# Performance work log

Hardware: AMD Instinct MI355X
Metric: run time of the kernel (lower is better)

The kernel has to match this reference:

```python
import jax, jax.numpy as jnp
import numpy as np

B, D, NH, HD = 32, 384, 8, 48
HP = WP = 14
N = HP * WP
L = 24
EPS_LN = 1e-5


def _ln(x, w, b):
    m = jnp.mean(x, -1, keepdims=True)
    v = jnp.mean((x - m) ** 2, -1, keepdims=True)
    return (x - m) * jax.lax.rsqrt(v + EPS_LN) * w + b


def _gelu(x):
    return jax.nn.gelu(x, approximate=False)


def _conv(x, w, s, p, groups=1):
    return jax.lax.conv_general_dilated(x, w, (s, s), [(p, p), (p, p)],
        dimension_numbers=('NCHW', 'OIHW', 'NCHW'), feature_group_count=groups)


def _bn(x, g, b):
    # eval-mode BatchNorm2d with running_mean=0, running_var=1
    scale = g * jax.lax.rsqrt(jnp.asarray(1.0 + 1e-5, x.dtype))
    return x * scale[None, :, None, None] + b[None, :, None, None]


def _pos_embed(pos_w, pos_b):
    two_pi = 2.0 * np.pi
    y = (jnp.arange(HP, dtype=jnp.float32) + 1.0) / ((HP + 1e-6) * two_pi)
    xg = (jnp.arange(WP, dtype=jnp.float32) + 1.0) / ((WP + 1e-6) * two_pi)
    y_embed = jnp.broadcast_to(y[:, None], (HP, WP))
    x_embed = jnp.broadcast_to(xg[None, :], (HP, WP))
    dim_t = 10000.0 ** (2.0 * (jnp.arange(32) // 2).astype(jnp.float32) / 32.0)
    px = x_embed[..., None] / dim_t  # [H,W,32]
    py = y_embed[..., None] / dim_t
    px = jnp.stack([jnp.sin(px[..., 0::2]), jnp.cos(px[..., 1::2])], -1).reshape(HP, WP, 32)
    py = jnp.stack([jnp.sin(py[..., 0::2]), jnp.cos(py[..., 1::2])], -1).reshape(HP, WP, 32)
    pos = jnp.concatenate([py, px], -1)  # [H,W,64]
    pos = jnp.einsum('hwc,dc->hwd', pos, pos_w[:, :, 0, 0]) + pos_b
    return pos.reshape(1, N, D)


def _xca_block(t, p):
    Bc = t.shape[0]
    h = _ln(t, p['n1_w'], p['n1_b'])
    qkv = (h @ p['qkv_w'].T + p['qkv_b']).reshape(Bc, N, 3, NH, HD)
    q = qkv[:, :, 0].transpose(0, 2, 3, 1)  # [B,H,d,N]
    k = qkv[:, :, 1].transpose(0, 2, 3, 1)
    v = qkv[:, :, 2].transpose(0, 2, 3, 1)
    q = q / jnp.maximum(jnp.linalg.norm(q, axis=-1, keepdims=True), 1e-12)
    k = k / jnp.maximum(jnp.linalg.norm(k, axis=-1, keepdims=True), 1e-12)
    attn = jnp.einsum('bhdn,bhen->bhde', q, k) * p['temp'][None, :, None, None]
    a = jax.nn.softmax(attn, -1)  # channel-wise softmax over d_h
    o = jnp.einsum('bhde,bhen->bnhd', a, v).reshape(Bc, N, D)
    o = o @ p['proj_w'].T + p['proj_b']
    t = t + p['g1'] * o
    h = _ln(t, p['n3_w'], p['n3_b']).transpose(0, 2, 1).reshape(Bc, D, HP, WP)
    h = _conv(h, p['lpi1_w'], 1, 1, groups=D) + p['lpi1_b'][None, :, None, None]
    h = _bn(_gelu(h), p['lpi_bn_g'], p['lpi_bn_b'])
    h = _conv(h, p['lpi2_w'], 1, 1, groups=D) + p['lpi2_b'][None, :, None, None]
    t = t + p['g3'] * h.reshape(Bc, D, N).transpose(0, 2, 1)
    h = _ln(t, p['n2_w'], p['n2_b'])
    h = _gelu(h @ p['fc1_w'].T + p['fc1_b']) @ p['fc2_w'].T + p['fc2_b']
    return t + p['g2'] * h


def _ca_block(t, p):
    Bc, Nc, _ = t.shape
    h = _ln(t, p['n1_w'], p['n1_b'])
    qkv = (h @ p['qkv_w'].T + p['qkv_b']).reshape(Bc, Nc, 3, NH, HD)
    q = qkv[:, :, 0].transpose(0, 2, 1, 3)  # [B,H,N,d]
    k = qkv[:, :, 1].transpose(0, 2, 1, 3)
    v = qkv[:, :, 2].transpose(0, 2, 1, 3)
    attn = jnp.sum(q[:, :, :1] * k, -1) * (HD ** -0.5)  # [B,H,N]
    a = jax.nn.softmax(attn, -1)
    cls = jnp.einsum('bhn,bhnd->bhd', a, v).reshape(Bc, 1, D)
    cls = cls @ p['proj_w'].T + p['proj_b']
    attn_out = jnp.concatenate([cls, h[:, 1:]], 1)
    t = t + p['g1'] * attn_out
    t = _ln(t, p['n2_w'], p['n2_b'])
    res = t
    cls2 = _gelu(t[:, :1] @ p['fc1_w'].T + p['fc1_b']) @ p['fc2_w'].T + p['fc2_b']
    return jnp.concatenate([p['g2'] * cls2, t[:, 1:]], 1) + res


def setup_inputs() -> dict:
    key = jax.random.key(0)
    k = iter(jax.random.split(key, 64))
    def rn(shape, std=0.02):
        return jax.random.normal(next(k), shape, jnp.float32) * std
    inp = {}
    inp['x'] = jax.random.normal(next(k), (B, 3, 224, 224), jnp.float32)
    inp['cls_token'] = rn((1, 1, D))
    inp['pos_w'] = rn((D, 64, 1, 1))
    inp['pos_b'] = jnp.zeros((D,))
    for i, (co, ci) in enumerate([(48, 3), (96, 48), (192, 96), (384, 192)], 1):
        inp['pe_w%d' % i] = rn((co, ci, 3, 3))
        inp['pe_g%d' % i] = jnp.ones((co,))
        inp['pe_b%d' % i] = jnp.zeros((co,))
    inp['xqkv_w'] = rn((L, 3 * D, D)); inp['xqkv_b'] = jnp.zeros((L, 3 * D))
    inp['xproj_w'] = rn((L, D, D)); inp['xproj_b'] = jnp.zeros((L, D))
    inp['xtemp'] = jnp.ones((L, NH))
    for n in ('n1', 'n2', 'n3'):
        inp['x%s_w' % n] = jnp.ones((L, D)); inp['x%s_b' % n] = jnp.zeros((L, D))
    inp['xfc1_w'] = rn((L, 4 * D, D)); inp['xfc1_b'] = jnp.zeros((L, 4 * D))
    inp['xfc2_w'] = rn((L, D, 4 * D)); inp['xfc2_b'] = jnp.zeros((L, D))
    inp['xlpi1_w'] = rn((L, D, 1, 3, 3), 0.1); inp['xlpi1_b'] = jnp.zeros((L, D))
    inp['xlpi2_w'] = rn((L, D, 1, 3, 3), 0.1); inp['xlpi2_b'] = jnp.zeros((L, D))
    inp['xbn_g'] = jnp.ones((L, D)); inp['xbn_b'] = jnp.zeros((L, D))
    for g in ('g1', 'g2', 'g3'):
        inp['x%s' % g] = jnp.full((L, D), 1e-5)
    L2 = 2
    inp['cqkv_w'] = rn((L2, 3 * D, D)); inp['cqkv_b'] = jnp.zeros((L2, 3 * D))
    inp['cproj_w'] = rn((L2, D, D)); inp['cproj_b'] = jnp.zeros((L2, D))
    for n in ('n1', 'n2'):
        inp['c%s_w' % n] = jnp.ones((L2, D)); inp['c%s_b' % n] = jnp.zeros((L2, D))
    inp['cfc1_w'] = rn((L2, 4 * D, D)); inp['cfc1_b'] = jnp.zeros((L2, 4 * D))
    inp['cfc2_w'] = rn((L2, D, 4 * D)); inp['cfc2_b'] = jnp.zeros((L2, D))
    inp['cg1'] = jnp.full((L2, D), 1e-5); inp['cg2'] = jnp.full((L2, D), 1e-5)
    inp['norm_w'] = jnp.ones((D,)); inp['norm_b'] = jnp.zeros((D,))
    inp['head_w'] = rn((1000, D)); inp['head_b'] = jnp.zeros((1000,))
    return inp


def reference(x, cls_token, pos_w, pos_b, pe_w1, pe_g1, pe_b1, pe_w2, pe_g2, pe_b2, pe_w3, pe_g3, pe_b3, pe_w4, pe_g4, pe_b4, xqkv_w, xqkv_b, xproj_w, xproj_b, xtemp, xn1_w, xn1_b, xn2_w, xn2_b, xn3_w, xn3_b, xfc1_w, xfc1_b, xfc2_w, xfc2_b, xlpi1_w, xlpi1_b, xlpi2_w, xlpi2_b, xbn_g, xbn_b, xg1, xg2, xg3, cqkv_w, cqkv_b, cproj_w, cproj_b, cn1_w, cn1_b, cn2_w, cn2_b, cfc1_w, cfc1_b, cfc2_w, cfc2_b, cg1, cg2, norm_w, norm_b, head_w, head_b):
    h = _gelu(_bn(_conv(x, pe_w1, 2, 1), pe_g1, pe_b1))
    h = _gelu(_bn(_conv(h, pe_w2, 2, 1), pe_g2, pe_b2))
    h = _gelu(_bn(_conv(h, pe_w3, 2, 1), pe_g3, pe_b3))
    h = _bn(_conv(h, pe_w4, 2, 1), pe_g4, pe_b4)  # [B,D,14,14]
    t = h.reshape(h.shape[0], D, N).transpose(0, 2, 1)  # [B,N,D]
    t = t + _pos_embed(pos_w, pos_b)
    xca = {'qkv_w': xqkv_w, 'qkv_b': xqkv_b, 'proj_w': xproj_w, 'proj_b': xproj_b,
           'temp': xtemp, 'n1_w': xn1_w, 'n1_b': xn1_b, 'n2_w': xn2_w, 'n2_b': xn2_b,
           'n3_w': xn3_w, 'n3_b': xn3_b, 'fc1_w': xfc1_w, 'fc1_b': xfc1_b,
           'fc2_w': xfc2_w, 'fc2_b': xfc2_b, 'lpi1_w': xlpi1_w, 'lpi1_b': xlpi1_b,
           'lpi2_w': xlpi2_w, 'lpi2_b': xlpi2_b, 'lpi_bn_g': xbn_g, 'lpi_bn_b': xbn_b,
           'g1': xg1, 'g2': xg2, 'g3': xg3}
    t, _ = jax.lax.scan(lambda c, p: (_xca_block(c, p), None), t, xca)
    t = jnp.concatenate([jnp.broadcast_to(cls_token, (t.shape[0], 1, D)), t], 1)
    for i in range(2):
        p = {'qkv_w': cqkv_w[i], 'qkv_b': cqkv_b[i], 'proj_w': cproj_w[i],
             'proj_b': cproj_b[i], 'n1_w': cn1_w[i], 'n1_b': cn1_b[i],
             'n2_w': cn2_w[i], 'n2_b': cn2_b[i], 'fc1_w': cfc1_w[i],
             'fc1_b': cfc1_b[i], 'fc2_w': cfc2_w[i], 'fc2_b': cfc2_b[i],
             'g1': cg1[i], 'g2': cg2[i]}
        t = _ca_block(t, p)
    t = _ln(t, norm_w, norm_b)[:, 0]
    return t @ head_w.T + head_b
```

## Files before the change

### kernel.cpp

```cpp
#include <hip/hip_runtime.h>
#include <hip/hip_bf16.h>

#define B_ 32
#define D_ 384
#define N_ 196
#define NH_ 8
#define HD_ 48
#define L_ 24

typedef __bf16 bf16x8 __attribute__((ext_vector_type(8)));
typedef __bf16 bf16x4 __attribute__((ext_vector_type(4)));
typedef float f32x4 __attribute__((ext_vector_type(4)));

__device__ __forceinline__ float gelu_f(float v){
    return 0.5f * v * (1.0f + erff(v * 0.70710678118654752f));
}

__global__ __launch_bounds__(256) void cvt_bf(const float* __restrict__ s, __bf16* __restrict__ d, long n){
    long i = ((long)blockIdx.x * 256 + threadIdx.x) * 8;
    if (i >= n) return;
    float4 a = *reinterpret_cast<const float4*>(s + i);
    float4 b = *reinterpret_cast<const float4*>(s + i + 4);
    bf16x8 r;
    r[0] = (__bf16)a.x; r[1] = (__bf16)a.y; r[2] = (__bf16)a.z; r[3] = (__bf16)a.w;
    r[4] = (__bf16)b.x; r[5] = (__bf16)b.y; r[6] = (__bf16)b.z; r[7] = (__bf16)b.w;
    *reinterpret_cast<bf16x8*>(d + i) = r;
}

__global__ __launch_bounds__(256) void cvt_pad(const float* __restrict__ s, __bf16* __restrict__ d,
                                               int rows, int K, int rows_pad){
    int id = blockIdx.x * 256 + threadIdx.x;
    if (id >= rows_pad * K) return;
    int r = id / K;
    d[id] = (r < rows) ? (__bf16)s[id] : (__bf16)0.f;
}

__global__ __launch_bounds__(256) void wprep(const float* __restrict__ w, __bf16* __restrict__ W2,
                                             int Co, int Ci, int Kpad){
    int id = blockIdx.x * 256 + threadIdx.x;
    if (id >= Co * Kpad) return;
    int co = id / Kpad, k = id - co * Kpad;
    float v = 0.f;
    if (k < 9 * Ci){
        int tap = k / Ci, ci = k - tap * Ci;
        v = w[((long)co * Ci + ci) * 9 + tap];
    }
    W2[id] = (__bf16)v;
}

__global__ __launch_bounds__(256) void im2col_x(const float* __restrict__ x, __bf16* __restrict__ A){
    int id = blockIdx.x * 256 + threadIdx.x;
    if (id >= 401408) return;
    int ox = id % 112; int t1 = id / 112; int oy = t1 % 112; int b = t1 / 112;
    __bf16 buf[32];
    #pragma unroll
    for (int i = 0; i < 32; i++) buf[i] = (__bf16)0.f;
    const float* xb = x + (long)b * 3 * 224 * 224;
    #pragma unroll
    for (int tap = 0; tap < 9; tap++){
        int ky = tap / 3, kx = tap % 3;
        int iy = oy * 2 - 1 + ky, ix = ox * 2 - 1 + kx;
        if ((unsigned)iy < 224u && (unsigned)ix < 224u){
            #pragma unroll
            for (int ci = 0; ci < 3; ci++)
                buf[tap * 3 + ci] = (__bf16)xb[((long)ci * 224 + iy) * 224 + ix];
        }
    }
    __bf16* dst = A + (long)id * 32;
    #pragma unroll
    for (int i = 0; i < 4; i++)
        *reinterpret_cast<bf16x8*>(dst + i * 8) = *reinterpret_cast<bf16x8*>(buf + i * 8);
}

__global__ __launch_bounds__(256) void im2col_bf(const __bf16* __restrict__ in, __bf16* __restrict__ A,
                                                 int C, int Hi, int Wi, int Ho, int Wo, int Kpad, int total){
    int id = blockIdx.x * 256 + threadIdx.x;
    if (id >= total) return;
    int tap = id % 9; int pix = id / 9;
    int ox = pix % Wo; int t1 = pix / Wo; int oy = t1 % Ho; int b = t1 / Ho;
    int ky = tap / 3, kx = tap % 3;
    int iy = oy * 2 - 1 + ky, ix = ox * 2 - 1 + kx;
    __bf16* dst = A + (long)pix * Kpad + tap * C;
    if ((unsigned)iy < (unsigned)Hi && (unsigned)ix < (unsigned)Wi){
        const __bf16* src = in + ((long)(b * Hi + iy) * Wi + ix) * C;
        for (int c = 0; c < C; c += 8)
            *reinterpret_cast<bf16x8*>(dst + c) = *reinterpret_cast<const bf16x8*>(src + c);
    } else {
        bf16x8 z{};
        for (int c = 0; c < C; c += 8) *reinterpret_cast<bf16x8*>(dst + c) = z;
    }
    if (tap == 0){
        bf16x8 z{};
        for (int c = 9 * C; c < Kpad; c += 8)
            *reinterpret_cast<bf16x8*>(A + (long)pix * Kpad + c) = z;
    }
}

template<int GELU, int POSOUT>
__global__ __launch_bounds__(256) void gemm_conv(const __bf16* __restrict__ A, int Kpad,
                                                 const __bf16* __restrict__ W,
                                                 const float* __restrict__ g, const float* __restrict__ bb,
                                                 void* __restrict__ Cv, int N,
                                                 const float* __restrict__ pos){
    __shared__ __align__(16) char smem[20480];
    char* Ab = smem;
    char* Bb = smem + 10240;
    const int tid  = threadIdx.x;
    const int lane = tid & 63;
    const int wn   = (tid >> 6) & 1;
    const int wm   = tid >> 7;
    const int row0 = blockIdx.x * 128;
    const int col0 = blockIdx.y * 128;
    const int hi = lane >> 4, lo = lane & 15;
    f32x4 acc[4][4] = {};
    auto loadA = [&](int kk, int i)->bf16x8 {
        int p = i * 256 + tid;
        int r = p >> 2, cq = p & 3;
        return *reinterpret_cast<const bf16x8*>(A + (long)(row0 + r) * Kpad + kk + cq * 8);
    };
    auto loadB = [&](int kk, int i)->bf16x8 {
        int p = i * 256 + tid;
        int r = p >> 2, cq = p & 3;
        int gc = col0 + r;
        bf16x8 vw{};
        if (gc < N) vw = *reinterpret_cast<const bf16x8*>(W + (long)gc * Kpad + kk + cq * 8);
        return vw;
    };
    bf16x8 vaC0 = loadA(0, 0), vaC1 = loadA(0, 1);
    bf16x8 vwC0 = loadB(0, 0), vwC1 = loadB(0, 1);
    for (int k0 = 0; k0 < Kpad; k0 += 32){
        #pragma unroll
        for (int i = 0; i < 2; i++){
            int p = i * 256 + tid;
            int r = p >> 2, cq = p & 3;
            *reinterpret_cast<bf16x8*>(Ab + r * 80 + cq * 16) = i ? vaC1 : vaC0;
            *reinterpret_cast<bf16x8*>(Bb + r * 80 + cq * 16) = i ? vwC1 : vwC0;
        }
        __syncthreads();
        int kn = (k0 + 32 < Kpad) ? k0 + 32 : k0;
        bf16x8 vaN0 = loadA(kn, 0), vaN1 = loadA(kn, 1);
        bf16x8 vwN0 = loadB(kn, 0), vwN1 = loadB(kn, 1);
        bf16x8 af[4], bfr[4];
        #pragma unroll
        for (int m = 0; m < 4; m++)
            af[m] = *reinterpret_cast<const bf16x8*>(Ab + (wm * 64 + m * 16 + lo) * 80 + hi * 16);
        #pragma unroll
        for (int n = 0; n < 4; n++)
            bfr[n] = *reinterpret_cast<const bf16x8*>(Bb + (wn * 64 + n * 16 + lo) * 80 + hi * 16);
        #pragma unroll
        for (int m = 0; m < 4; m++)
            #pragma unroll
            for (int n = 0; n < 4; n++)
                acc[m][n] = __builtin_amdgcn_mfma_f32_16x16x32_bf16(af[m], bfr[n], acc[m][n], 0, 0, 0);
        __syncthreads();
        vaC0 = vaN0; vaC1 = vaN1; vwC0 = vwN0; vwC1 = vwN1;
    }
    float* Cf = (float*)Cv;
    __bf16* Cb = (__bf16*)Cv;
    #pragma unroll
    for (int m = 0; m < 4; m++){
        #pragma unroll
        for (int n = 0; n < 4; n++){
            int row = row0 + wm * 64 + m * 16 + hi * 4;
            int col = col0 + wn * 64 + n * 16 + lo;
            if (col >= N) continue;
            float scale = g[col] * rsqrtf(1.0f + 1e-5f);
            float bv = bb[col];
            #pragma unroll
            for (int j = 0; j < 4; j++){
                float v = acc[m][n][j] * scale + bv;
                if (GELU) v = gelu_f(v);
                if (POSOUT)
                    Cf[(long)(row + j) * 384 + col] = v + pos[((row + j) % 196) * 384 + col];
                else
                    Cb[(long)(row + j) * N + col] = (__bf16)v;
            }
        }
    }
}

__global__ __launch_bounds__(128) void ln384(const float* __restrict__ x, long xstride,
                                             const float* __restrict__ w, const float* __restrict__ b,
                                             float* __restrict__ y, long ystride){
    long row = blockIdx.x;
    int tid = threadIdx.x;
    const float* xr = x + row * xstride;
    float v0 = xr[tid], v1 = xr[tid + 128], v2 = xr[tid + 256];
    float s = v0 + v1 + v2;
    float ss = v0 * v0 + v1 * v1 + v2 * v2;
    for (int off = 32; off; off >>= 1){ s += __shfl_down(s, off); ss += __shfl_down(ss, off); }
    __shared__ float rs[2], rss[2];
    if ((tid & 63) == 0){ rs[tid >> 6] = s; rss[tid >> 6] = ss; }
    __syncthreads();
    float S = rs[0] + rs[1], SS = rss[0] + rss[1];
    float m = S * (1.0f / 384.0f);
    float var = SS * (1.0f / 384.0f) - m * m;
    float r = rsqrtf(var + 1e-5f);
    float* yr = y + row * ystride;
    yr[tid]       = (v0 - m) * r * w[tid]       + b[tid];
    yr[tid + 128] = (v1 - m) * r * w[tid + 128] + b[tid + 128];
    yr[tid + 256] = (v2 - m) * r * w[tid + 256] + b[tid + 256];
}

__global__ __launch_bounds__(128) void ln384_bf(const float* __restrict__ x,
                                                const float* __restrict__ w, const float* __restrict__ b,
                                                __bf16* __restrict__ y){
    long row = blockIdx.x;
    int tid = threadIdx.x;
    const float* xr = x + row * 384;
    float v0 = xr[tid], v1 = xr[tid + 128], v2 = xr[tid + 256];
    float s = v0 + v1 + v2;
    float ss = v0 * v0 + v1 * v1 + v2 * v2;
    for (int off = 32; off; off >>= 1){ s += __shfl_down(s, off); ss += __shfl_down(ss, off); }
    __shared__ float rs[2], rss[2];
    if ((tid & 63) == 0){ rs[tid >> 6] = s; rss[tid >> 6] = ss; }
    __syncthreads();
    float S = rs[0] + rs[1], SS = rss[0] + rss[1];
    float m = S * (1.0f / 384.0f);
    float var = SS * (1.0f / 384.0f) - m * m;
    float r = rsqrtf(var + 1e-5f);
    __bf16* yr = y + row * 384;
    yr[tid]       = (__bf16)((v0 - m) * r * w[tid]       + b[tid]);
    yr[tid + 128] = (__bf16)((v1 - m) * r * w[tid + 128] + b[tid + 128]);
    yr[tid + 256] = (__bf16)((v2 - m) * r * w[tid + 256] + b[tid + 256]);
}

__global__ __launch_bounds__(128) void proj_res_lnt(const __bf16* __restrict__ o2,
                                                    const float* __restrict__ g1,
                                                    float* __restrict__ t,
                                                    const float* __restrict__ n3w, const float* __restrict__ n3b,
                                                    __bf16* __restrict__ ht){
    long row = blockIdx.x;
    int tid = threadIdx.x;
    int c0 = tid * 4;
    float v[4] = {0.f, 0.f, 0.f, 0.f};
    if (tid < 96){
        float4 tv = *reinterpret_cast<const float4*>(t + row * 384 + c0);
        bf16x4 ov = *reinterpret_cast<const bf16x4*>(o2 + row * 384 + c0);
        v[0] = tv.x + g1[c0 + 0] * (float)ov[0];
        v[1] = tv.y + g1[c0 + 1] * (float)ov[1];
        v[2] = tv.z + g1[c0 + 2] * (float)ov[2];
        v[3] = tv.w + g1[c0 + 3] * (float)ov[3];
        *reinterpret_cast<float4*>(t + row * 384 + c0) = make_float4(v[0], v[1], v[2], v[3]);
    }
    float s = v[0] + v[1] + v[2] + v[3];
    float ss = v[0] * v[0] + v[1] * v[1] + v[2] * v[2] + v[3] * v[3];
    for (int off = 32; off; off >>= 1){ s += __shfl_down(s, off); ss += __shfl_down(ss, off); }
    __shared__ float rs[2], rss[2];
    if ((tid & 63) == 0){ rs[tid >> 6] = s; rss[tid >> 6] = ss; }
    __syncthreads();
    float S = rs[0] + rs[1], SS = rss[0] + rss[1];
    float m = S * (1.0f / 384.0f);
    float var = SS * (1.0f / 384.0f) - m * m;
    float r = rsqrtf(var + 1e-5f);
    if (tid < 96){
        int b = (int)(row / 196), n = (int)(row % 196);
        __bf16* yb = ht + ((long)b * 384) * 196 + n;
        #pragma unroll
        for (int j = 0; j < 4; j++){
            int c = c0 + j;
            yb[(long)c * 196] = (__bf16)((v[j] - m) * r * n3w[c] + n3b[c]);
        }
    }
}

__global__ __launch_bounds__(128) void ln2res(float* __restrict__ t,
                                              const __bf16* __restrict__ hadd,
                                              const float* __restrict__ n2w, const float* __restrict__ n2b,
                                              __bf16* __restrict__ h){
    long row = blockIdx.x;
    int tid = threadIdx.x;
    int c0 = tid * 4;
    float v[4] = {0.f, 0.f, 0.f, 0.f};
    if (tid < 96){
        float4 tv = *reinterpret_cast<const float4*>(t + row * 384 + c0);
        bf16x4 hv = *reinterpret_cast<const bf16x4*>(hadd + row * 384 + c0);
        v[0] = tv.x + (float)hv[0];
        v[1] = tv.y + (float)hv[1];
        v[2] = tv.z + (float)hv[2];
        v[3] = tv.w + (float)hv[3];
        *reinterpret_cast<float4*>(t + row * 384 + c0) = make_float4(v[0], v[1], v[2], v[3]);
    }
    float s = v[0] + v[1] + v[2] + v[3];
    float ss = v[0] * v[0] + v[1] * v[1] + v[2] * v[2] + v[3] * v[3];
    for (int off = 32; off; off >>= 1){ s += __shfl_down(s, off); ss += __shfl_down(ss, off); }
    __shared__ float rs[2], rss[2];
    if ((tid & 63) == 0){ rs[tid >> 6] = s; rss[tid >> 6] = ss; }
    __syncthreads();
    float S = rs[0] + rs[1], SS = rss[0] + rss[1];
    float m = S * (1.0f / 384.0f);
    float var = SS * (1.0f / 384.0f) - m * m;
    float r = rsqrtf(var + 1e-5f);
    if (tid < 96){
        bf16x4 o;
        #pragma unroll
        for (int j = 0; j < 4; j++){
            int c = c0 + j;
            o[j] = (__bf16)((v[j] - m) * r * n2w[c] + n2b[c]);
        }
        *reinterpret_cast<bf16x4*>(h + row * 384 + c0) = o;
    }
}

__global__ __launch_bounds__(128) void fc2_res_ln(const __bf16* __restrict__ f2,
                                                  const float* __restrict__ g2,
                                                  float* __restrict__ t,
                                                  const float* __restrict__ n1w, const float* __restrict__ n1b,
                                                  __bf16* __restrict__ h){
    long row = blockIdx.x;
    int tid = threadIdx.x;
    int c0 = tid * 4;
    float v[4] = {0.f, 0.f, 0.f, 0.f};
    if (tid < 96){
        float4 tv = *reinterpret_cast<const float4*>(t + row * 384 + c0);
        bf16x4 fv = *reinterpret_cast<const bf16x4*>(f2 + row * 384 + c0);
        v[0] = tv.x + g2[c0 + 0] * (float)fv[0];
        v[1] = tv.y + g2[c0 + 1] * (float)fv[1];
        v[2] = tv.z + g2[c0 + 2] * (float)fv[2];
        v[3] = tv.w + g2[c0 + 3] * (float)fv[3];
        *reinterpret_cast<float4*>(t + row * 384 + c0) = make_float4(v[0], v[1], v[2], v[3]);
    }
    float s = v[0] + v[1] + v[2] + v[3];
    float ss = v[0] * v[0] + v[1] * v[1] + v[2] * v[2] + v[3] * v[3];
    for (int off = 32; off; off >>= 1){ s += __shfl_down(s, off); ss += __shfl_down(ss, off); }
    __shared__ float rs[2], rss[2];
    if ((tid & 63) == 0){ rs[tid >> 6] = s; rss[tid >> 6] = ss; }
    __syncthreads();
    float S = rs[0] + rs[1], SS = rss[0] + rss[1];
    float m = S * (1.0f / 384.0f);
    float var = SS * (1.0f / 384.0f) - m * m;
    float r = rsqrtf(var + 1e-5f);
    if (tid < 96){
        bf16x4 o;
        #pragma unroll
        for (int j = 0; j < 4; j++){
            int c = c0 + j;
            o[j] = (__bf16)((v[j] - m) * r * n1w[c] + n1b[c]);
        }
        *reinterpret_cast<bf16x4*>(h + row * 384 + c0) = o;
    }
}

template<int MODE, int OUTBF, int ACVT, int GUARD, int NGUARD>
__global__ __launch_bounds__(256) void gemm_bb2(const void* __restrict__ Av, long lda,
                                                const __bf16* __restrict__ W, int Kw,
                                                const float* __restrict__ bias,
                                                void* __restrict__ Cv, long ldc,
                                                int K, int M, int Ncols){
    __shared__ __align__(16) char smem[27648];
    char* Ab = smem;
    char* Bb = smem + 9216;
    const int tid = threadIdx.x;
    const int lane = tid & 63;
    const int wn = tid >> 6;
    const int row0 = blockIdx.x * 64;
    const int col0 = blockIdx.y * 128;
    const int hi = lane >> 4, lo = lane & 15;
    const __bf16* Abf = (const __bf16*)Av;
    const float* Af = (const float*)Av;
    f32x4 acc[4][2] = {};
    auto loadA = [&](int kk, int i)->bf16x8 {
        int p = i * 256 + tid;
        int r = p >> 3, cq = p & 7;
        bf16x8 va{};
        int grow = row0 + r;
        if (!GUARD || grow < M){
            long ai = (long)grow * lda + kk + cq * 8;
            if (ACVT){
                float4 a0 = *reinterpret_cast<const float4*>(Af + ai);
                float4 a1 = *reinterpret_cast<const float4*>(Af + ai + 4);
                va[0] = (__bf16)a0.x; va[1] = (__bf16)a0.y; va[2] = (__bf16)a0.z; va[3] = (__bf16)a0.w;
                va[4] = (__bf16)a1.x; va[5] = (__bf16)a1.y; va[6] = (__bf16)a1.z; va[7] = (__bf16)a1.w;
            } else {
                va = *reinterpret_cast<const bf16x8*>(Abf + ai);
            }
        }
        return va;
    };
    auto loadB = [&](int kk, int i)->bf16x8 {
        int p = i * 256 + tid;
        int r = p >> 3, cq = p & 7;
        return *reinterpret_cast<const bf16x8*>(W + (long)(col0 + r) * Kw + kk + cq * 8);
    };
    bf16x8 vaC[2], vwC[4];
    vaC[0] = loadA(0, 0); vaC[1] = loadA(0, 1);
    #pragma unroll
    for (int i = 0; i < 4; i++) vwC[i] = loadB(0, i);
    for (int k0 = 0; k0 < K; k0 += 64){
        #pragma unroll
        for (int i = 0; i < 2; i++){
            int p = i * 256 + tid;
            int r = p >> 3, cq = p & 7;
            *reinterpret_cast<bf16x8*>(Ab + r * 144 + cq * 16) = vaC[i];
        }
        #pragma unroll
        for (int i = 0; i < 4; i++){
            int p = i * 256 + tid;
            int r = p >> 3, cq = p & 7;
            *reinterpret_cast<bf16x8*>(Bb + r * 144 + cq * 16) = vwC[i];
        }
        __syncthreads();
        int kn = (k0 + 64 < K) ? k0 + 64 : k0;
        bf16x8 vaN[2], vwN[4];
        vaN[0] = loadA(kn, 0); vaN[1] = loadA(kn, 1);
        #pragma unroll
        for (int i = 0; i < 4; i++) vwN[i] = loadB(kn, i);
        bf16x8 af[2][4], bfr[2][2];
        #pragma unroll
        for (int m = 0; m < 4; m++){
            af[0][m] = *reinterpret_cast<const bf16x8*>(Ab + (m * 16 + lo) * 144 + hi * 16);
            af[1][m] = *reinterpret_cast<const bf16x8*>(Ab + (m * 16 + lo) * 144 + 64 + hi * 16);
        }
        #pragma unroll
        for (int n = 0; n < 2; n++){
            bfr[0][n] = *reinterpret_cast<const bf16x8*>(Bb + (wn * 32 + n * 16 + lo) * 144 + hi * 16);
            bfr[1][n] = *reinterpret_cast<const bf16x8*>(Bb + (wn * 32 + n * 16 + lo) * 144 + 64 + hi * 16);
        }
        #pragma unroll
        for (int kc = 0; kc < 2; kc++)
            #pragma unroll
            for (int m = 0; m < 4; m++)
                #pragma unroll
                for (int n = 0; n < 2; n++)
                    acc[m][n] = __builtin_amdgcn_mfma_f32_16x16x32_bf16(af[kc][m], bfr[kc][n], acc[m][n], 0, 0, 0);
        __syncthreads();
        vaC[0] = vaN[0]; vaC[1] = vaN[1];
        #pragma unroll
        for (int i = 0; i < 4; i++) vwC[i] = vwN[i];
    }
    float* Cf = (float*)Cv;
    __bf16* Cb = (__bf16*)Cv;
    #pragma unroll
    for (int m = 0; m < 4; m++){
        #pragma unroll
        for (int n = 0; n < 2; n++){
            int row = row0 + m * 16 + hi * 4;
            int col = col0 + wn * 32 + n * 16 + lo;
            if (NGUARD && col >= Ncols) continue;
            float bv = bias[col];
            #pragma unroll
            for (int j = 0; j < 4; j++){
                if (GUARD && (row + j) >= M) continue;
                float v = acc[m][n][j] + bv;
                if (MODE == 1) v = gelu_f(v);
                long ci = (long)(row + j) * ldc + col;
                if (OUTBF) Cb[ci] = (__bf16)v;
                else Cf[ci] = v;
            }
        }
    }
}

__global__ __launch_bounds__(256) void gemm_bb3(const __bf16* __restrict__ A, long lda,
                                                const __bf16* __restrict__ W, int Kw,
                                                const float* __restrict__ bias,
                                                __bf16* __restrict__ C, long ldc,
                                                int K){
    __shared__ __align__(16) char smem[18432];
// ... 126 lines not shown
    __syncthreads();
    for (int r = wid; r < 48; r += 4){
        float sq = 0.f, sk = 0.f;
        for (int n = lane; n < 196; n += 64){
            float qv = (float)qs[r * 232 + n];
            float kv = (float)ks[r * 232 + n];
            sq += qv * qv; sk += kv * kv;
        }
        for (int off = 32; off; off >>= 1){ sq += __shfl_down(sq, off); sk += __shfl_down(sk, off); }
        if (lane == 0){
            inq[r] = 1.0f / fmaxf(sqrtf(sq), 1e-12f);
            ink[r] = 1.0f / fmaxf(sqrtf(sk), 1e-12f);
        }
    }
    __syncthreads();
    float tempv = temp[h];
    f32x4 qk0 = {}, qk1 = {}, qk2 = {};
    __builtin_amdgcn_s_setprio(1);
    {
        int mi = wid / 3, ni = wid % 3;
        #pragma unroll
        for (int k0 = 0; k0 < 224; k0 += 32){
            bf16x8 af = *reinterpret_cast<const bf16x8*>(qs + (mi * 16 + lo) * 232 + k0 + hi * 8);
            bf16x8 bf = *reinterpret_cast<const bf16x8*>(ks + (ni * 16 + lo) * 232 + k0 + hi * 8);
            qk0 = __builtin_amdgcn_mfma_f32_16x16x32_bf16(af, bf, qk0, 0, 0, 0);
        }
    }
    {
        int tt = wid + 4;
        int mi = tt / 3, ni = tt % 3;
        #pragma unroll
        for (int k0 = 0; k0 < 224; k0 += 32){
            bf16x8 af = *reinterpret_cast<const bf16x8*>(qs + (mi * 16 + lo) * 232 + k0 + hi * 8);
            bf16x8 bf = *reinterpret_cast<const bf16x8*>(ks + (ni * 16 + lo) * 232 + k0 + hi * 8);
            qk1 = __builtin_amdgcn_mfma_f32_16x16x32_bf16(af, bf, qk1, 0, 0, 0);
        }
    }
    if (wid == 0){
        #pragma unroll
        for (int k0 = 0; k0 < 224; k0 += 32){
            bf16x8 af = *reinterpret_cast<const bf16x8*>(qs + (2 * 16 + lo) * 232 + k0 + hi * 8);
            bf16x8 bf = *reinterpret_cast<const bf16x8*>(ks + (2 * 16 + lo) * 232 + k0 + hi * 8);
            qk2 = __builtin_amdgcn_mfma_f32_16x16x32_bf16(af, bf, qk2, 0, 0, 0);
        }
    }
    __builtin_amdgcn_s_setprio(0);
    __syncthreads();
    {
        int mi = wid / 3, ni = wid % 3;
        int e = ni * 16 + lo;
        float se = ink[e] * tempv;
        #pragma unroll
        for (int j = 0; j < 4; j++){
            int d = mi * 16 + hi * 4 + j;
            att[d * 68 + e] = qk0[j] * inq[d] * se;
        }
    }
    {
        int tt = wid + 4;
        int mi = tt / 3, ni = tt % 3;
        int e = ni * 16 + lo;
        float se = ink[e] * tempv;
        #pragma unroll
        for (int j = 0; j < 4; j++){
            int d = mi * 16 + hi * 4 + j;
            att[d * 68 + e] = qk1[j] * inq[d] * se;
        }
    }
    if (wid == 0){
        int e = 2 * 16 + lo;
        float se = ink[e] * tempv;
        #pragma unroll
        for (int j = 0; j < 4; j++){
            int d = 2 * 16 + hi * 4 + j;
            att[d * 68 + e] = qk2[j] * inq[d] * se;
        }
    }
    __syncthreads();
    if (tid < 192){
        int r = tid >> 2, q4 = tid & 3;
        const float* row = att + r * 68 + q4 * 12;
        float mx = -1e30f;
        #pragma unroll
        for (int i = 0; i < 12; i++) mx = fmaxf(mx, row[i]);
        mx = fmaxf(mx, __shfl_xor(mx, 1));
        mx = fmaxf(mx, __shfl_xor(mx, 2));
        float pv[12]; float sm = 0.f;
        #pragma unroll
        for (int i = 0; i < 12; i++){ pv[i] = expf(row[i] - mx); sm += pv[i]; }
        sm += __shfl_xor(sm, 1);
        sm += __shfl_xor(sm, 2);
        float inv = 1.0f / sm;
        #pragma unroll
        for (int i = 0; i < 12; i++) abf[r * 72 + q4 * 12 + i] = (__bf16)(pv[i] * inv);
    }
    for (int idx = tid; idx < 48 * 3; idx += 256){
        int r = idx / 3, c = 48 + (idx % 3) * 8;
        *reinterpret_cast<bf16x8*>(abf + r * 72 + c) = z8;
    }
    __syncthreads();
    __bf16* ob = o + ((long)b * 196) * 384 + h * 48;
    __builtin_amdgcn_s_setprio(1);
    for (int tt = wid; tt < 39; tt += 4){
        int mi = tt / 13, ni = tt % 13;
        int nB = ni * 16 + lo;
        const __bf16* vrow = base + (long)nB * 1152 + 768;
        f32x4 acc = {};
        #pragma unroll
        for (int e0 = 0; e0 < 64; e0 += 32){
            bf16x8 af = *reinterpret_cast<const bf16x8*>(abf + (mi * 16 + lo) * 72 + e0 + hi * 8);
            bf16x8 bf = *reinterpret_cast<const bf16x8*>(vrow + e0 + hi * 8);
            acc = __builtin_amdgcn_mfma_f32_16x16x32_bf16(af, bf, acc, 0, 0, 0);
        }
        int n = nB;
        if (n < 196){
            #pragma unroll
            for (int j = 0; j < 4; j++){
                int d = mi * 16 + hi * 4 + j;
                ob[(long)n * 384 + d] = (__bf16)acc[j];
            }
        }
    }
    __builtin_amdgcn_s_setprio(0);
}

__global__ __launch_bounds__(256) void lpi_g(const __bf16* __restrict__ ht,
                                             const float* __restrict__ w1, const float* __restrict__ b1,
                                             const float* __restrict__ bng, const float* __restrict__ bnb,
                                             const float* __restrict__ w2, const float* __restrict__ b2,
                                             const float* __restrict__ g3, __bf16* __restrict__ hadd){
    int bd = blockIdx.x;
    int d = bd % 384, b = bd / 384;
    __shared__ float p[16][16];
    __shared__ float p2[16][16];
    __shared__ float wA[9], wB[9];
    int tt = threadIdx.x;
    int yy = tt / 16, xx = tt % 16;
    p[yy][xx] = 0.f; p2[yy][xx] = 0.f;
    if (tt < 9){ wA[tt] = w1[d * 9 + tt]; wB[tt] = w2[d * 9 + tt]; }
    __syncthreads();
    if (tt < 196){
        int y = tt / 14, x = tt % 14;
        p[y + 1][x + 1] = (float)ht[((long)b * 384 + d) * 196 + tt];
    }
    __syncthreads();
    if (tt < 196){
        int y = tt / 14, x = tt % 14;
        float a = 0.f;
        #pragma unroll
        for (int ky = 0; ky < 3; ky++)
            #pragma unroll
            for (int kx = 0; kx < 3; kx++)
                a += wA[ky * 3 + kx] * p[y + ky][x + kx];
        a += b1[d];
        a = gelu_f(a);
        a = a * (bng[d] * rsqrtf(1.0f + 1e-5f)) + bnb[d];
        p2[y + 1][x + 1] = a;
    }
    __syncthreads();
    if (tt < 196){
        int y = tt / 14, x = tt % 14;
        float a = 0.f;
        #pragma unroll
        for (int ky = 0; ky < 3; ky++)
            #pragma unroll
            for (int kx = 0; kx < 3; kx++)
                a += wB[ky * 3 + kx] * p2[y + ky][x + kx];
        a += b2[d];
        hadd[((long)b * 196 + tt) * 384 + d] = (__bf16)(g3[d] * a);
    }
}

__global__ __launch_bounds__(256) void concat_cls(const float* __restrict__ t, const float* __restrict__ clstok,
                                                  float* __restrict__ tc){
    long i = (long)blockIdx.x * 256 + threadIdx.x;
    if (i >= (long)B_ * 197 * 384) return;
    int d = (int)(i % 384);
    long bn = i / 384;
    int n = (int)(bn % 197);
    int b = (int)(bn / 197);
    tc[i] = (n == 0) ? clstok[d] : t[((long)b * 196 + (n - 1)) * 384 + d];
}

__global__ __launch_bounds__(256) void ca_attn(const __bf16* __restrict__ qkv, float* __restrict__ clsp){
    int bh = blockIdx.x;
    int b = bh >> 3, h = bh & 7;
    const __bf16* base = qkv + (long)b * 197 * 1152 + h * 48;
    __shared__ float q0[48];
    __shared__ float at2[197];
    __shared__ float smax, ssum;
    int tid = threadIdx.x;
    if (tid < 48) q0[tid] = (float)base[tid];
    __syncthreads();
    if (tid < 197){
        const __bf16* kr = base + (long)tid * 1152 + 384;
        float s = 0.f;
        for (int d = 0; d < 48; d++) s += q0[d] * (float)kr[d];
        at2[tid] = s * rsqrtf(48.0f);
    }
    __syncthreads();
    if (tid == 0){
        float m = -1e30f;
        for (int n = 0; n < 197; n++) m = fmaxf(m, at2[n]);
        smax = m;
    }
    __syncthreads();
    if (tid < 197) at2[tid] = expf(at2[tid] - smax);
    __syncthreads();
    if (tid == 0){
        float s = 0.f;
        for (int n = 0; n < 197; n++) s += at2[n];
        ssum = s;
    }
    __syncthreads();
    if (tid < 48){
        const __bf16* vb = base + 768 + tid;
        float s = 0.f;
        for (int n = 0; n < 197; n++) s += at2[n] * (float)vb[(long)n * 1152];
        clsp[b * 384 + h * 48 + tid] = s / ssum;
    }
}

__global__ __launch_bounds__(256) void ca_update1(const float* __restrict__ clso, const float* __restrict__ hc,
                                                  const float* __restrict__ g1, float* __restrict__ tc){
    long i = (long)blockIdx.x * 256 + threadIdx.x;
    if (i >= (long)B_ * 197 * 384) return;
    int d = (int)(i % 384);
    long bn = i / 384;
    int n = (int)(bn % 197);
    int b = (int)(bn / 197);
    float add = (n == 0) ? clso[b * 384 + d] : hc[i];
    tc[i] += g1[d] * add;
}

__global__ __launch_bounds__(256) void ca_update2(const float* __restrict__ cls2, const float* __restrict__ hc,
                                                  const float* __restrict__ g2, float* __restrict__ tc){
    long i = (long)blockIdx.x * 256 + threadIdx.x;
    if (i >= (long)B_ * 197 * 384) return;
    int d = (int)(i % 384);
    long bn = i / 384;
    int n = (int)(bn % 197);
    int b = (int)(bn / 197);
    float hv = hc[i];
    tc[i] = (n == 0) ? (g2[d] * cls2[b * 384 + d] + hv) : (hv + hv);
}

extern "C" void kernel_launch(void* const* d_in, const int* in_sizes, int n_in,
                              void* d_out, int out_size, void* d_ws, size_t ws_size,
                              hipStream_t stream){
    (void)in_sizes; (void)n_in; (void)out_size; (void)ws_size;
    const float* x      = (const float*)d_in[0];
    const float* clstok = (const float*)d_in[1];
    const float* pos_w  = (const float*)d_in[2];
    const float* pos_b  = (const float*)d_in[3];
    const float* pe_w[4] = {(const float*)d_in[4], (const float*)d_in[7], (const float*)d_in[10], (const float*)d_in[13]};
    const float* pe_g[4] = {(const float*)d_in[5], (const float*)d_in[8], (const float*)d_in[11], (const float*)d_in[14]};
    const float* pe_b[4] = {(const float*)d_in[6], (const float*)d_in[9], (const float*)d_in[12], (const float*)d_in[15]};
    const float* xqkv_w = (const float*)d_in[16];
    const float* xqkv_b = (const float*)d_in[17];
    const float* xproj_w = (const float*)d_in[18];
    const float* xproj_b = (const float*)d_in[19];
    const float* xtemp  = (const float*)d_in[20];
    const float* xn1_w = (const float*)d_in[21];
    const float* xn1_b = (const float*)d_in[22];
    const float* xn2_w = (const float*)d_in[23];
    const float* xn2_b = (const float*)d_in[24];
    const float* xn3_w = (const float*)d_in[25];
    const float* xn3_b = (const float*)d_in[26];
    const float* xfc1_w = (const float*)d_in[27];
    const float* xfc1_b = (const float*)d_in[28];
    const float* xfc2_w = (const float*)d_in[29];
    const float* xfc2_b = (const float*)d_in[30];
    const float* xlpi1_w = (const float*)d_in[31];
    const float* xlpi1_b = (const float*)d_in[32];
    const float* xlpi2_w = (const float*)d_in[33];
    const float* xlpi2_b = (const float*)d_in[34];
    const float* xbn_g = (const float*)d_in[35];
    const float* xbn_b = (const float*)d_in[36];
    const float* xg1 = (const float*)d_in[37];
    const float* xg2 = (const float*)d_in[38];
    const float* xg3 = (const float*)d_in[39];
    const float* cqkv_w = (const float*)d_in[40];
    const float* cqkv_b = (const float*)d_in[41];
    const float* cproj_w = (const float*)d_in[42];
    const float* cproj_b = (const float*)d_in[43];
    const float* cn1_w = (const float*)d_in[44];
    const float* cn1_b = (const float*)d_in[45];
    const float* cn2_w = (const float*)d_in[46];
    const float* cn2_b = (const float*)d_in[47];
    const float* cfc1_w = (const float*)d_in[48];
    const float* cfc1_b = (const float*)d_in[49];
    const float* cfc2_w = (const float*)d_in[50];
    const float* cfc2_b = (const float*)d_in[51];
    const float* cg1 = (const float*)d_in[52];
    const float* cg2 = (const float*)d_in[53];
    const float* norm_w = (const float*)d_in[54];
    const float* norm_b = (const float*)d_in[55];
    const float* head_w = (const float*)d_in[56];
    const float* head_b = (const float*)d_in[57];
    float* outp = (float*)d_out;

    float* ws = (float*)d_ws;
    __bf16* A1   = (__bf16*)(ws);
    __bf16* A2   = (__bf16*)(ws);
    __bf16* A3   = (__bf16*)(ws);
    __bf16* A4   = (__bf16*)(ws);
    __bf16* out1 = (__bf16*)(ws + 22500000L);
    __bf16* out2 = (__bf16*)(ws + 22500000L);
    __bf16* out3 = (__bf16*)(ws + 27400000L);
    __bf16* wcv  = (__bf16*)(ws + 36000000L);
    __bf16* W1c = wcv;
    __bf16* W2c = wcv + 1536;
    __bf16* W3c = wcv + 44544;
    __bf16* W4c = wcv + 216576;
    __bf16* wqkv_bf = (__bf16*)(ws);
    __bf16* wproj_bf = (__bf16*)(ws + 5308416L);
    __bf16* wfc1_bf = (__bf16*)(ws + 7077888L);
    __bf16* wfc2_bf = (__bf16*)(ws + 14155776L);
    float*  t       = ws + 21233664L;
    float*  pos     = ws + 23642112L;
    __bf16* h_bf    = (__bf16*)(ws + 23717376L);
    __bf16* qkv_bf  = (__bf16*)(ws + 24921600L);
    __bf16* o_bf    = (__bf16*)(ws + 28534272L);
    __bf16* ht_bf   = (__bf16*)(ws + 29738496L);
    __bf16* f1_bf   = (__bf16*)(ws + 32146944L);
    __bf16* o2_bf   = (__bf16*)(ws + 34555392L);
    __bf16* f2_bf   = (__bf16*)(ws + 24921600L);
    __bf16* hadd_bf = (__bf16*)(ws + 28534272L);
    float* tc   = ws;
    float* hc   = ws + 2420736L;
    __bf16* qkvc_bf = (__bf16*)(ws + 4841472L);
    float* clsp = ws + 8472576L;
    float* clso = clsp + 12288;
    float* f1c  = clso + 12288;
    float* cls2 = f1c + 49152;
    float* clsf = cls2 + 12288;
    __bf16* cqkv_bf  = (__bf16*)(ws + 9000000L);
    __bf16* cproj_bf = (__bf16*)(ws + 9500000L);
    __bf16* cfc1_bf  = (__bf16*)(ws + 9800000L);
    __bf16* cfc2_bf  = (__bf16*)(ws + 10400000L);
    __bf16* headw_bf = (__bf16*)(ws + 11000000L);

    wprep<<<(48 * 32 + 255) / 256, 256, 0, stream>>>(pe_w[0], W1c, 48, 3, 32);
    wprep<<<(96 * 448 + 255) / 256, 256, 0, stream>>>(pe_w[1], W2c, 96, 48, 448);
    wprep<<<(192 * 896 + 255) / 256, 256, 0, stream>>>(pe_w[2], W3c, 192, 96, 896);
    wprep<<<(384 * 1728 + 255) / 256, 256, 0, stream>>>(pe_w[3], W4c, 384, 192, 1728);

    im2col_x<<<1568, 256, 0, stream>>>(x, A1);
    { dim3 g(3136, 1); gemm_conv<1, 0><<<g, 256, 0, stream>>>(A1, 32, W1c, pe_g[0], pe_b[0], out1, 48, nullptr); }
    im2col_bf<<<(100352 * 9 + 255) / 256, 256, 0, stream>>>(out1, A2, 48, 112, 112, 56, 56, 448, 100352 * 9);
    { dim3 g(784, 1); gemm_conv<1, 0><<<g, 256, 0, stream>>>(A2, 448, W2c, pe_g[1], pe_b[1], out2, 96, nullptr); }
    im2col_bf<<<(25088 * 9 + 255) / 256, 256, 0, stream>>>(out2, A3, 96, 56, 56, 28, 28, 896, 25088 * 9);
    pos_embed<<<196, 384, 0, stream>>>(pos_w, pos_b, pos);
    { dim3 g(196, 2); gemm_conv<1, 0><<<g, 256, 0, stream>>>(A3, 896, W3c, pe_g[2], pe_b[2], out3, 192, nullptr); }
    im2col_bf<<<(6272 * 9 + 255) / 256, 256, 0, stream>>>(out3, A4, 192, 28, 28, 14, 14, 1728, 6272 * 9);
    { dim3 g(49, 3); gemm_conv<0, 1><<<g, 256, 0, stream>>>(A4, 1728, W4c, pe_g[3], pe_b[3], t, 384, pos); }

    {
        long n1 = (long)L_ * 1152 * 384;
        long n2 = (long)L_ * 384 * 384;
        long n3 = (long)L_ * 1536 * 384;
        cvt_bf<<<(int)((n1 + 2047) / 2048), 256, 0, stream>>>(xqkv_w, wqkv_bf, n1);
        cvt_bf<<<(int)((n2 + 2047) / 2048), 256, 0, stream>>>(xproj_w, wproj_bf, n2);
        cvt_bf<<<(int)((n3 + 2047) / 2048), 256, 0, stream>>>(xfc1_w, wfc1_bf, n3);
        cvt_bf<<<(int)((n3 + 2047) / 2048), 256, 0, stream>>>(xfc2_w, wfc2_bf, n3);
    }

    const int M = B_ * N_;
    ln384_bf<<<M, 128, 0, stream>>>(t, xn1_w, xn1_b, h_bf);
    for (int l = 0; l < L_; l++){
        {
            dim3 g(98, 9);
            gemm_bb2<0, 1, 0, 0, 0><<<g, 256, 0, stream>>>(h_bf, 384, wqkv_bf + (long)l * 1152 * 384, 384,
                                                           xqkv_b + l * 1152, qkv_bf, 1152, 384, M, 0);
        }
        xca2<<<B_ * NH_, 256, 0, stream>>>(qkv_bf, xtemp + l * 8, o_bf);
        {
            dim3 g(98, 6);
            gemm_bb3<<<g, 256, 0, stream>>>(o_bf, 384, wproj_bf + (long)l * 384 * 384, 384,
                                            xproj_b + l * 384, o2_bf, 384, 384);
        }
        proj_res_lnt<<<M, 128, 0, stream>>>(o2_bf, xg1 + l * 384, t,
                                            xn3_w + l * 384, xn3_b + l * 384, ht_bf);
        lpi_g<<<B_ * D_, 256, 0, stream>>>(ht_bf, xlpi1_w + (long)l * 384 * 9, xlpi1_b + l * 384,
                                           xbn_g + l * 384, xbn_b + l * 384,
                                           xlpi2_w + (long)l * 384 * 9, xlpi2_b + l * 384,
                                           xg3 + l * 384, hadd_bf);
        ln2res<<<M, 128, 0, stream>>>(t, hadd_bf, xn2_w + l * 384, xn2_b + l * 384, h_bf);
        {
            dim3 g(98, 12);
            gemm_bb2<1, 1, 0, 0, 0><<<g, 256, 0, stream>>>(h_bf, 384, wfc1_bf + (long)l * 1536 * 384, 384,
                                                           xfc1_b + l * 1536, f1_bf, 1536, 384, M, 0);
        }
        {
            dim3 g(98, 6);
            gemm_bb3<<<g, 256, 0, stream>>>(f1_bf, 1536, wfc2_bf + (long)l * 1536 * 384, 1536,
                                            xfc2_b + l * 384, f2_bf, 384, 1536);
        }
        int ln = (l + 1) % L_;
        fc2_res_ln<<<M, 128, 0, stream>>>(f2_bf, xg2 + l * 384, t,
                                          xn1_w + ln * 384, xn1_b + ln * 384, h_bf);
    }

    const long NC = (long)B_ * 197 * 384;
    concat_cls<<<(int)(NC / 256), 256, 0, stream>>>(t, clstok, tc);
    {
        long nc = (long)2 * 1152 * 384;
        cvt_bf<<<(int)((nc + 2047) / 2048), 256, 0, stream>>>(cqkv_w, cqkv_bf, nc);
        long np = (long)2 * 384 * 384;
        cvt_bf<<<(int)((np + 2047) / 2048), 256, 0, stream>>>(cproj_w, cproj_bf, np);
        long nf = (long)2 * 1536 * 384;
        cvt_bf<<<(int)((nf + 2047) / 2048), 256, 0, stream>>>(cfc1_w, cfc1_bf, nf);
        cvt_bf<<<(int)((nf + 2047) / 2048), 256, 0, stream>>>(cfc2_w, cfc2_bf, nf);
        cvt_pad<<<(1024 * 384 + 255) / 256, 256, 0, stream>>>(head_w, headw_bf, 1000, 384, 1024);
    }
    const int MC = B_ * 197;
    for (int i = 0; i < 2; i++){
        ln384<<<MC, 128, 0, stream>>>(tc, 384, cn1_w + i * 384, cn1_b + i * 384, hc, 384);
        {
            dim3 g(99, 9);
            gemm_bb2<0, 1, 1, 1, 0><<<g, 256, 0, stream>>>(hc, 384, cqkv_bf + (long)i * 1152 * 384, 384,
                                                           cqkv_b + i * 1152, qkvc_bf, 1152, 384, MC, 0);
        }
        ca_attn<<<B_ * NH_, 256, 0, stream>>>(qkvc_bf, clsp);
        {
            dim3 g(1, 3);
            gemm_bb2<0, 0, 1, 1, 0><<<g, 256, 0, stream>>>(clsp, 384, cproj_bf + (long)i * 384 * 384, 384,
                                                           cproj_b + i * 384, clso, 384, 384, 32, 0);
        }
        ca_update1<<<(int)(NC / 256), 256, 0, stream>>>(clso, hc, cg1 + i * 384, tc);
        ln384<<<MC, 128, 0, stream>>>(tc, 384, cn2_w + i * 384, cn2_b + i * 384, hc, 384);
        {
            dim3 g(1, 12);
            gemm_bb2<1, 0, 1, 1, 0><<<g, 256, 0, stream>>>(hc, (long)197 * 384, cfc1_bf + (long)i * 1536 * 384, 384,
                                                           cfc1_b + i * 1536, f1c, 1536, 384, 32, 0);
        }
        {
            dim3 g(1, 3);
            gemm_bb2<0, 0, 1, 1, 0><<<g, 256, 0, stream>>>(f1c, 1536, cfc2_bf + (long)i * 1536 * 384, 1536,
                                                           cfc2_b + i * 384, cls2, 384, 1536, 32, 0);
        }
        ca_update2<<<(int)(NC / 256), 256, 0, stream>>>(cls2, hc, cg2 + i * 384, tc);
    }

    ln384<<<32, 128, 0, stream>>>(tc, (long)197 * 384, norm_w, norm_b, clsf, 384);
    {
        dim3 g(1, 8);
        gemm_bb2<0, 0, 1, 1, 1><<<g, 256, 0, stream>>>(clsf, 384, headw_bf, 384,
                                                       head_b, outp, 1000, 384, 32, 1000);
    }
}
```

Baseline: 3.932 ms.

## Fuse im2col into patch-embed conv GEMMs via implicit-GEMM gather

Replaces the separate im2col kernels for conv layers 2-4 with an implicit-GEMM kernel that gathers 3x3 stride-2 patches directly from the NHWC bf16 activations while loading A tiles. This removes writing and re-reading large im2col buffers to global memory. The new kernel also uses a 64-wide K step with more loads in flight per thread, at the cost of extra index arithmetic and more shared memory per block.

After: 3.778 ms. 3.9% less time.

```diff
diff --git a/kernel.cpp b/kernel.cpp
--- a/kernel.cpp
+++ b/kernel.cpp
@@ -70,30 +70,6 @@
     #pragma unroll
     for (int i = 0; i < 4; i++)
         *reinterpret_cast<bf16x8*>(dst + i * 8) = *reinterpret_cast<bf16x8*>(buf + i * 8);
-}
-
-__global__ __launch_bounds__(256) void im2col_bf(const __bf16* __restrict__ in, __bf16* __restrict__ A,
-                                                 int C, int Hi, int Wi, int Ho, int Wo, int Kpad, int total){
-    int id = blockIdx.x * 256 + threadIdx.x;
-    if (id >= total) return;
-    int tap = id % 9; int pix = id / 9;
-    int ox = pix % Wo; int t1 = pix / Wo; int oy = t1 % Ho; int b = t1 / Ho;
-    int ky = tap / 3, kx = tap % 3;
-    int iy = oy * 2 - 1 + ky, ix = ox * 2 - 1 + kx;
-    __bf16* dst = A + (long)pix * Kpad + tap * C;
-    if ((unsigned)iy < (unsigned)Hi && (unsigned)ix < (unsigned)Wi){
-        const __bf16* src = in + ((long)(b * Hi + iy) * Wi + ix) * C;
-        for (int c = 0; c < C; c += 8)
-            *reinterpret_cast<bf16x8*>(dst + c) = *reinterpret_cast<const bf16x8*>(src + c);
-    } else {
-        bf16x8 z{};
-        for (int c = 0; c < C; c += 8) *reinterpret_cast<bf16x8*>(dst + c) = z;
-    }
-    if (tap == 0){
-        bf16x8 z{};
-        for (int c = 9 * C; c < Kpad; c += 8)
-            *reinterpret_cast<bf16x8*>(A + (long)pix * Kpad + c) = z;
-    }
 }
 
 template<int GELU, int POSOUT>
@@ -154,6 +130,111 @@
                 acc[m][n] = __builtin_amdgcn_mfma_f32_16x16x32_bf16(af[m], bfr[n], acc[m][n], 0, 0, 0);
         __syncthreads();
         vaC0 = vaN0; vaC1 = vaN1; vwC0 = vwN0; vwC1 = vwN1;
+    }
+    float* Cf = (float*)Cv;
+    __bf16* Cb = (__bf16*)Cv;
+    #pragma unroll
+    for (int m = 0; m < 4; m++){
+        #pragma unroll
+        for (int n = 0; n < 4; n++){
+            int row = row0 + wm * 64 + m * 16 + hi * 4;
+            int col = col0 + wn * 64 + n * 16 + lo;
+            if (col >= N) continue;
+            float scale = g[col] * rsqrtf(1.0f + 1e-5f);
+            float bv = bb[col];
+            #pragma unroll
+            for (int j = 0; j < 4; j++){
+                float v = acc[m][n][j] * scale + bv;
+                if (GELU) v = gelu_f(v);
+                if (POSOUT)
+                    Cf[(long)(row + j) * 384 + col] = v + pos[((row + j) % 196) * 384 + col];
+                else
+                    Cb[(long)(row + j) * N + col] = (__bf16)v;
+            }
+        }
+    }
+}
+
+template<int GELU, int POSOUT, int C, int Hi, int Wi, int Ho, int Wo>
+__global__ __launch_bounds__(256) void gemm_cig(const __bf16* __restrict__ in, int Kpad,
+                                                const __bf16* __restrict__ W,
+                                                const float* __restrict__ g, const float* __restrict__ bb,
+                                                void* __restrict__ Cv, int N,
+                                                const float* __restrict__ pos){
+    __shared__ __align__(16) char smem[36864];
+    char* Ab = smem;
+    char* Bb = smem + 18432;
+    const int tid  = threadIdx.x;
+    const int lane = tid & 63;
+    const int wn   = (tid >> 6) & 1;
+    const int wm   = tid >> 7;
+    const int row0 = blockIdx.x * 128;
+    const int col0 = blockIdx.y * 128;
+    const int hi = lane >> 4, lo = lane & 15;
+    f32x4 acc[4][4] = {};
+    auto loadA = [&](int kk, int i)->bf16x8 {
+        int p = i * 256 + tid;
+        int r = p >> 3, cq = p & 7;
+        int koff = kk + cq * 8;
+        int tap = koff / C;
+        int ci = koff - tap * C;
+        bf16x8 va{};
+        if (tap < 9){
+            int pix = row0 + r;
+            int b = pix / (Ho * Wo);
+            int rem = pix - b * (Ho * Wo);
+            int oy = rem / Wo, ox = rem - oy * Wo;
+            int iy = oy * 2 - 1 + tap / 3, ix = ox * 2 - 1 + tap % 3;
+            if ((unsigned)iy < (unsigned)Hi && (unsigned)ix < (unsigned)Wi)
+                va = *reinterpret_cast<const bf16x8*>(in + (((long)b * Hi + iy) * Wi + ix) * C + ci);
+        }
+        return va;
+    };
+    auto loadB = [&](int kk, int i)->bf16x8 {
+        int p = i * 256 + tid;
+        int r = p >> 3, cq = p & 7;
+        int gc = col0 + r;
+        bf16x8 vw{};
+        if (gc < N) vw = *reinterpret_cast<const bf16x8*>(W + (long)gc * Kpad + kk + cq * 8);
+        return vw;
+    };
+    bf16x8 vaC[4], vwC[4];
+    #pragma unroll
+    for (int i = 0; i < 4; i++){ vaC[i] = loadA(0, i); vwC[i] = loadB(0, i); }
+    for (int k0 = 0; k0 < Kpad; k0 += 64){
+        #pragma unroll
+        for (int i = 0; i < 4; i++){
+            int p = i * 256 + tid;
+            int r = p >> 3, cq = p & 7;
+            *reinterpret_cast<bf16x8*>(Ab + r * 144 + cq * 16) = vaC[i];
+            *reinterpret_cast<bf16x8*>(Bb + r * 144 + cq * 16) = vwC[i];
+        }
+        __syncthreads();
+        int kn = (k0 + 64 < Kpad) ? k0 + 64 : k0;
+        bf16x8 vaN[4], vwN[4];
+        #pragma unroll
+        for (int i = 0; i < 4; i++){ vaN[i] = loadA(kn, i); vwN[i] = loadB(kn, i); }
+        bf16x8 af[2][4], bfr[2][4];
+        #pragma unroll
+        for (int m = 0; m < 4; m++){
+            af[0][m] = *reinterpret_cast<const bf16x8*>(Ab + (wm * 64 + m * 16 + lo) * 144 + hi * 16);
+            af[1][m] = *reinterpret_cast<const bf16x8*>(Ab + (wm * 64 + m * 16 + lo) * 144 + 64 + hi * 16);
+        }
+        #pragma unroll
+        for (int n = 0; n < 4; n++){
+            bfr[0][n] = *reinterpret_cast<const bf16x8*>(Bb + (wn * 64 + n * 16 + lo) * 144 + hi * 16);
+            bfr[1][n] = *reinterpret_cast<const bf16x8*>(Bb + (wn * 64 + n * 16 + lo) * 144 + 64 + hi * 16);
+        }
+        #pragma unroll
+        for (int kc = 0; kc < 2; kc++)
+            #pragma unroll
+            for (int m = 0; m < 4; m++)
+                #pragma unroll
+                for (int n = 0; n < 4; n++)
+                    acc[m][n] = __builtin_amdgcn_mfma_f32_16x16x32_bf16(af[kc][m], bfr[kc][n], acc[m][n], 0, 0, 0);
+        __syncthreads();
+        #pragma unroll
+        for (int i = 0; i < 4; i++){ vaC[i] = vaN[i]; vwC[i] = vwN[i]; }
     }
     float* Cf = (float*)Cv;
     __bf16* Cb = (__bf16*)Cv;
@@ -886,12 +967,9 @@
 
     float* ws = (float*)d_ws;
     __bf16* A1   = (__bf16*)(ws);
-    __bf16* A2   = (__bf16*)(ws);
-    __bf16* A3   = (__bf16*)(ws);
-    __bf16* A4   = (__bf16*)(ws);
-    __bf16* out1 = (__bf16*)(ws + 22500000L);
-    __bf16* out2 = (__bf16*)(ws + 22500000L);
-    __bf16* out3 = (__bf16*)(ws + 27400000L);
+    __bf16* out1 = (__bf16*)(ws + 7000000L);
+    __bf16* out2 = (__bf16*)(ws + 17000000L);
+    __bf16* out3 = (__bf16*)(ws + 25000000L);
     __bf16* wcv  = (__bf16*)(ws + 36000000L);
     __bf16* W1c = wcv;
     __bf16* W2c = wcv + 1536;
@@ -932,13 +1010,13 @@
 
     im2col_x<<<1568, 256, 0, stream>>>(x, A1);
     { dim3 g(3136, 1); gemm_conv<1, 0><<<g, 256, 0, stream>>>(A1, 32, W1c, pe_g[0], pe_b[0], out1, 48, nullptr); }
-    im2col_bf<<<(100352 * 9 + 255) / 256, 256, 0, stream>>>(out1, A2, 48, 112, 112, 56, 56, 448, 100352 * 9);
-    { dim3 g(784, 1); gemm_conv<1, 0><<<g, 256, 0, stream>>>(A2, 448, W2c, pe_g[1], pe_b[1], out2, 96, nullptr); }
-    im2col_bf<<<(25088 * 9 + 255) / 256, 256, 0, stream>>>(out2, A3, 96, 56, 56, 28, 28, 896, 25088 * 9);
     pos_embed<<<196, 384, 0, stream>>>(pos_w, pos_b, pos);
-    { dim3 g(196, 2); gemm_conv<1, 0><<<g, 256, 0, stream>>>(A3, 896, W3c, pe_g[2], pe_b[2], out3, 192, nullptr); }
-    im2col_bf<<<(6272 * 9 + 255) / 256, 256, 0, stream>>>(out3, A4, 192, 28, 28, 14, 14, 1728, 6272 * 9);
-    { dim3 g(49, 3); gemm_conv<0, 1><<<g, 256, 0, stream>>>(A4, 1728, W4c, pe_g[3], pe_b[3], t, 384, pos); }
+    { dim3 g(784, 1);
+      gemm_cig<1, 0, 48, 112, 112, 56, 56><<<g, 256, 0, stream>>>(out1, 448, W2c, pe_g[1], pe_b[1], out2, 96, nullptr); }
+    { dim3 g(196, 2);
+      gemm_cig<1, 0, 96, 56, 56, 28, 28><<<g, 256, 0, stream>>>(out2, 896, W3c, pe_g[2], pe_b[2], out3, 192, nullptr); }
+    { dim3 g(49, 3);
+      gemm_cig<0, 1, 192, 28, 28, 14, 14><<<g, 256, 0, stream>>>(out3, 1728, W4c, pe_g[3], pe_b[3], t, 384, pos); }
 
     {
         long n1 = (long)L_ * 1152 * 384;
```
